# Optimization experiments

Hardware: AMD Instinct MI355X
Metric: run time of the kernel (lower is better)

The kernel has to match this reference:

```python
import jax, jax.numpy as jnp
import numpy as np

LMAX_IN = 3
LMAX_OUT = 3
C = 64          # num_channel
H = 64          # num_channel_hidden
N_NODES = 2048
N_EDGES = 8192

# All coupled (l1, l2, l3) paths with |l1-l2| <= l3 <= min(l1+l2, lmax_out)
COMBS = [(l1, l2, l3)
         for l1 in range(LMAX_IN + 1)
         for l2 in range(LMAX_OUT + 1)
         for l3 in range(abs(l1 - l2), min(l1 + l2, LMAX_OUT) + 1)]
COUNTS = {l3: sum(1 for c in COMBS if c[2] == l3) for l3 in range(LMAX_OUT + 1)}

# Fixed coupling (Clebsch-Gordan-like) tensors for each path, shape (2l1+1, 2l2+1, 2l3+1).
# Deterministic constants (not trained / not differentiated), standing in for the
# e3nn CG coefficients used by InterEinsumTC.
_rng = np.random.RandomState(1234)
CG = [jnp.asarray((_rng.randn(2 * l1 + 1, 2 * l2 + 1, 2 * l3 + 1) * 0.2).astype(np.float32))
      for (l1, l2, l3) in COMBS]


def setup_inputs() -> dict:
    key = jax.random.key(0)
    ks = jax.random.split(key, 16)
    inp = {}
    for l in range(LMAX_OUT + 1):
        inp[f"x{l}"] = jax.random.normal(ks[l], (N_NODES, C, 2 * l + 1), dtype=jnp.float32)
        inp[f"y{l}"] = jax.random.normal(ks[4 + l], (N_EDGES, 2 * l + 1), dtype=jnp.float32)
        fan_in = C * COUNTS[l]
        inp[f"w_lin{l}"] = jax.random.normal(ks[8 + l], (fan_in, H), dtype=jnp.float32) / np.float32(np.sqrt(fan_in))
    inp["ws"] = jax.random.normal(ks[12], (N_EDGES, C * len(COMBS)), dtype=jnp.float32)
    inp["edge_index"] = jax.random.randint(ks[13], (2, N_EDGES), 0, N_NODES, dtype=jnp.int32)
    return inp


def _forward(x0, x1, x2, x3, y0, y1, y2, y3, ws, w_lin0, w_lin1, w_lin2, w_lin3, edge_index):
    xs = (x0, x1, x2, x3)
    ys = (y0, y1, y2, y3)
    wl = (w_lin0, w_lin1, w_lin2, w_lin3)
    src, dst = edge_index[0], edge_index[1]
    # per-edge gather of node features for every input degree
    xg = [x[src] for x in xs]                      # [E, C, 2l1+1]
    buf = {l3: [] for l3 in range(LMAX_OUT + 1)}
    for i, (l1, l2, l3) in enumerate(COMBS):
        # tensor-product contraction: [E, C, 2l3+1]
        out = jnp.einsum('lmn,ecl,em->ecn', CG[i], xg[l1], ys[l2])
        w = ws[:, i * C:(i + 1) * C][:, :, None]   # [E, C, 1] per-path per-channel weight
        buf[l3].append(w * out)
    res = []
    for l3 in range(LMAX_OUT + 1):
        m_ji = jnp.concatenate(buf[l3], axis=1)    # [E, C*count_l3, 2l3+1]
        m_i = jax.ops.segment_sum(m_ji, dst, num_segments=N_NODES)  # scatter-sum -> [N, C*count, 2l3+1]
        res.append(jnp.einsum('ncm,ch->nhm', m_i, wl[l3]))          # per-l3 linear -> [N, H, 2l3+1]
    return tuple(res)


def reference(x0, x1, x2, x3, y0, y1, y2, y3, ws, w_lin0, w_lin1, w_lin2, w_lin3, edge_index):
    return _forward(x0, x1, x2, x3, y0, y1, y2, y3, ws,
                    w_lin0, w_lin1, w_lin2, w_lin3, edge_index)
```

## Files before the change

### kernel.cpp

```cpp
#include <hip/hip_runtime.h>
#include <hip/hip_bf16.h>
#include <cmath>
#include <cstdint>

#define NNODES 2048
#define NEDGES 8192
#define NCH 64
#define NHID 64
#define NPATH 34
#define NTASK (NPATH * NCH)
#define CGTOT 3436
#define MROW 9984
#define TT3 1028
#define EBLK 8
#define GLEN_MAX 564

#define MI_BYTES ((size_t)NNODES * MROW * 2)
#define XT_BYTES ((size_t)NNODES * 16 * NCH * 2)
#define WT_BYTES ((size_t)64 * NTASK * 2)
#define OFF_OFF  (MI_BYTES)
#define CUR_OFF  (OFF_OFF + 2052 * 4)
#define PACK_OFF (CUR_OFF + 2048 * 4)
#define ORD_OFF  (PACK_OFF + 8192 * 4)
#define XT_OFF   (ORD_OFF + 2048 * 4)
#define WT_OFF   (XT_OFF + XT_BYTES)
#define CGP_OFF  (WT_OFF + WT_BYTES)
#define CGP_FLOATS (TT3 * 9)

typedef __attribute__((ext_vector_type(8))) short short8;
typedef __attribute__((ext_vector_type(4))) float floatx4;

struct PathTables {
  int l1[NPATH], l2[NPATH], l3[NPATH];
  int cg_off[NPATH], t_off3[NPATH], rank[NPATH];
  int gpaths[2][20], gnp[2], gbase3[2], glen3[2];
  int cg_total, tt3, npaths;
};

constexpr PathTables make_tables() {
  PathTables tb{};
  int np = 0;
  for (int a = 0; a < 4; ++a)
    for (int b = 0; b < 4; ++b) {
      int lo = a > b ? a - b : b - a;
      int hi = a + b < 3 ? a + b : 3;
      for (int c = lo; c <= hi; ++c) { tb.l1[np] = a; tb.l2[np] = b; tb.l3[np] = c; ++np; }
    }
  int cg = 0;
  int cnt[4] = {0, 0, 0, 0};
  for (int i = 0; i < np; ++i) {
    tb.cg_off[i] = cg; tb.rank[i] = cnt[tb.l3[i]]++;
    cg += (2 * tb.l1[i] + 1) * (2 * tb.l2[i] + 1) * (2 * tb.l3[i] + 1);
  }
  int tt = 0;
  for (int g = 0; g < 2; ++g) {
    tb.gbase3[g] = tt;
    for (int i = 0; i < np; ++i) {
      int gi = (tb.l3[i] == 0 || tb.l3[i] == 3) ? 0 : 1;
      if (gi != g) continue;
      tb.gpaths[g][tb.gnp[g]++] = i;
      tb.t_off3[i] = tt;
      int d1 = 2 * tb.l1[i] + 1, d3 = 2 * tb.l3[i] + 1;
      int st = (d3 <= 4) ? 4 : 8;
      tt += d1 * st;
    }
    tb.glen3[g] = tt - tb.gbase3[g];
  }
  tb.cg_total = cg; tb.tt3 = tt; tb.npaths = np;
  return tb;
}

constexpr PathTables H_TB = make_tables();
static_assert(H_TB.npaths == NPATH, "npaths");
static_assert(H_TB.cg_total == CGTOT, "cgtot");
static_assert(H_TB.tt3 == TT3, "tt3");
static_assert(H_TB.gnp[0] == 14 && H_TB.gnp[1] == 20, "gnp");
static_assert(H_TB.gbase3[1] == 464 && H_TB.glen3[0] == 464 && H_TB.glen3[1] == 564, "gsplit");

__constant__ PathTables d_tb = make_tables();

namespace {
struct MT19937 {
  uint32_t mt[624]; int mti; bool has_g; double gval;
  void seed(uint32_t s) {
    for (int i = 0; i < 624; ++i) { mt[i] = s; s = 1812433253u * (s ^ (s >> 30)) + (uint32_t)i + 1u; }
    mti = 624; has_g = false; gval = 0.0;
  }
  uint32_t next() {
    if (mti >= 624) {
      for (int i = 0; i < 624; ++i) {
        uint32_t y = (mt[i] & 0x80000000u) | (mt[(i + 1) % 624] & 0x7fffffffu);
        mt[i] = mt[(i + 397) % 624] ^ (y >> 1) ^ ((y & 1u) ? 0x9908b0dfu : 0u);
      }
      mti = 0;
    }
    uint32_t y = mt[mti++];
    y ^= y >> 11; y ^= (y << 7) & 0x9d2c5680u; y ^= (y << 15) & 0xefc60000u; y ^= y >> 18;
    return y;
  }
  double rdbl() {
    uint32_t a = next() >> 5, b = next() >> 6;
    return ((double)a * 67108864.0 + (double)b) / 9007199254740992.0;
  }
  double gauss() {
    if (has_g) { has_g = false; return gval; }
    double x1, x2, r2;
    do {
      x1 = 2.0 * rdbl() - 1.0;
      x2 = 2.0 * rdbl() - 1.0;
      r2 = x1 * x1 + x2 * x2;
    } while (r2 >= 1.0 || r2 == 0.0);
    double f = std::sqrt(-2.0 * std::log(r2) / r2);
    gval = f * x1; has_g = true;
    return f * x2;
  }
};

float host_pack[CGP_FLOATS];
float* g_cg_dev = nullptr;
bool g_cg_ok = false;

struct CGInit {
  CGInit() {
    static float cg[CGTOT];
    MT19937 g; g.seed(1234u);
    int idx = 0;
    for (int i = 0; i < NPATH; ++i) {
      int d1 = 2 * H_TB.l1[i] + 1, d2 = 2 * H_TB.l2[i] + 1, d3 = 2 * H_TB.l3[i] + 1;
      int sz = d1 * d2 * d3;
      for (int k = 0; k < sz; ++k) cg[idx++] = (float)(g.gauss() * 0.2);
    }
    const int ybase[4] = {0, 1, 4, 9};
    for (int k = 0; k < CGP_FLOATS; ++k) host_pack[k] = 0.f;
    for (int i = 0; i < NPATH; ++i) {
      int d1 = 2 * H_TB.l1[i] + 1, d2 = 2 * H_TB.l2[i] + 1, d3 = 2 * H_TB.l3[i] + 1;
      int st = (d3 <= 4) ? 4 : 8;
      for (int l = 0; l < d1; ++l)
        for (int n3 = 0; n3 < d3; ++n3) {
          int slot = H_TB.t_off3[i] + l * st + n3;
          for (int m = 0; m < d2; ++m)
            host_pack[slot * 8 + m] = cg[H_TB.cg_off[i] + l * d2 * d3 + m * d3 + n3];
          host_pack[TT3 * 8 + slot] = (float)ybase[H_TB.l2[i]];
        }
    }
    (void)hipHostRegister(host_pack, sizeof(host_pack), hipHostRegisterDefault);
    void* p = nullptr;
    if (hipMalloc(&p, sizeof(host_pack)) == hipSuccess && p) {
      if (hipMemcpy(p, host_pack, sizeof(host_pack), hipMemcpyHostToDevice) == hipSuccess) {
        float back = -1.f;
        if (hipMemcpy(&back, (float*)p + (CGP_FLOATS - 1), sizeof(float),
                      hipMemcpyDeviceToHost) == hipSuccess && back == host_pack[CGP_FLOATS - 1]) {
          g_cg_dev = (float*)p;
          g_cg_ok = true;
        }
      }
    }
  }
} cg_init_instance;
}

__device__ __forceinline__ float bf2f(unsigned short u) {
  union { unsigned int i; float f; } v; v.i = ((unsigned int)u) << 16; return v.f;
}
__device__ __forceinline__ unsigned short f2bf(float f) {
  __hip_bfloat16 h = __float2bfloat16(f);
  union { __hip_bfloat16 h; unsigned short u; } v; v.h = h; return v.u;
}

__global__ __launch_bounds__(1024) void scan_kernel(
    const int* __restrict__ edge_index, int* __restrict__ off, int* __restrict__ cursor,
    int* __restrict__ order)
{
  __shared__ int ldeg[NNODES];
  __shared__ int csum[1024];
  __shared__ int hist[64];
  const int t = threadIdx.x;
  for (int i = t; i < NNODES; i += 1024) ldeg[i] = 0;
  __syncthreads();
  const int* __restrict__ dsts = edge_index + NEDGES;
  for (int e = t; e < NEDGES; e += 1024) atomicAdd(&ldeg[dsts[e]], 1);
  __syncthreads();
  const int l0 = ldeg[2 * t], l1 = ldeg[2 * t + 1];
  const int s = l0 + l1;
  csum[t] = s;
  __syncthreads();
  for (int o = 1; o < 1024; o <<= 1) {
    int v = (t >= o) ? csum[t - o] : 0;
    __syncthreads();
    csum[t] += v;
    __syncthreads();
  }
  int run = csum[t] - s;
  off[2 * t] = run; cursor[2 * t] = run;
  off[2 * t + 1] = run + l0; cursor[2 * t + 1] = run + l0;
  if (t == 0) off[NNODES] = NEDGES;
  if (t < 64) hist[t] = 0;
  __syncthreads();
  for (int i = t; i < NNODES; i += 1024) {
    int d = ldeg[i]; d = d > 63 ? 63 : d;
    atomicAdd(&hist[63 - d], 1);
  }
  __syncthreads();
  if (t == 0) { int r2 = 0; for (int b = 0; b < 64; ++b) { int c = hist[b]; hist[b] = r2; r2 += c; } }
  __syncthreads();
  for (int i = t; i < NNODES; i += 1024) {
    int d = ldeg[i]; d = d > 63 ? 63 : d;
    int pos = atomicAdd(&hist[63 - d], 1);
    order[pos] = i;
  }
}

__global__ __launch_bounds__(256) void fill_xt_kernel(
    const int* __restrict__ edge_index, int* __restrict__ cursor, int* __restrict__ pack,
    const float* __restrict__ x0, const float* __restrict__ x1,
    const float* __restrict__ x2, const float* __restrict__ x3,
    const float* __restrict__ wl0, const float* __restrict__ wl1,
    const float* __restrict__ wl2, const float* __restrict__ wl3,
    __hip_bfloat16* __restrict__ xT, unsigned short* __restrict__ wt_all)
{
  const int b = blockIdx.x;
  const int t = threadIdx.x;
  if (b < 32) {
    const int e = b * 256 + t;
    const int d = edge_index[NEDGES + e];
    const int s = edge_index[e];
    const int pos = atomicAdd(&cursor[d], 1);
    pack[pos] = e | (s << 13);
  } else if (b < 32 + NNODES) {
    const int n = b - 32;
    for (int idx = t; idx < 1024; idx += 256) {
      const int j = idx >> 6, c = idx & 63;
      const float* src; int d1, m;
      if (j < 1)      { src = x0; d1 = 1; m = j; }
      else if (j < 4) { src = x1; d1 = 3; m = j - 1; }
      else if (j < 9) { src = x2; d1 = 5; m = j - 4; }
      else            { src = x3; d1 = 7; m = j - 9; }
      const float v = src[((size_t)n * NCH + c) * d1 + m];
      xT[((size_t)n * 16 + j) * NCH + c] = __float2bfloat16(v);
    }
  } else {
    const int b3 = b - (32 + NNODES);
    const int k = b3 * 4 + (t >> 6);
    const int h = t & 63;
    const float* src; int K, base, kl;
    if (k < 256)       { src = wl0; K = 256; base = 0;     kl = k; }
    else if (k < 832)  { src = wl1; K = 576; base = 16384; kl = k - 256; }
    else if (k < 1536) { src = wl2; K = 704; base = 53248; kl = k - 832; }
    else               { src = wl3; K = 640; base = 98304; kl = k - 1536; }
    wt_all[base + h * K + kl] = f2bf(src[(size_t)kl * 64 + h]);
  }
}

template <int D1, int D3>
__device__ __forceinline__ void tp_task_run(
    int wcol, int toff_l, int rank, int nb, const int* __restrict__ epk,
    const float (*Ts)[GLEN_MAX], const float* __restrict__ ws,
    const unsigned short* __restrict__ xT,
    int n, bool first, __hip_bfloat16* __restrict__ m_out)
{
  constexpr int Kc = (D3 == 1) ? 256 : (D3 == 3) ? 576 : (D3 == 5) ? 704 : 640;
  constexpr int Rc = (D3 == 1) ? 0 : (D3 == 3) ? 256 : (D3 == 5) ? 1984 : 5504;
  constexpr int JB = (D1 == 1) ? 0 : (D1 == 3) ? 1 : (D1 == 5) ? 4 : 9;
  constexpr int ST = (D3 <= 4) ? 4 : 8;
  const int c = wcol & 63;

  float wv_[EBLK];
#pragma unroll
  for (int ei = 0; ei < EBLK; ++ei)
    wv_[ei] = (ei < nb) ? ws[(size_t)(epk[ei] & 8191) * NTASK + wcol] : 0.f;

  float acc[D3];
#pragma unroll
  for (int m = 0; m < D3; ++m) acc[m] = 0.f;

  for (int ei = 0; ei < nb; ++ei) {
    const int s = epk[ei] >> 13;
    const unsigned short* __restrict__ xr = xT + ((size_t)s * 16 + JB) * NCH + c;
    const float* __restrict__ Tp = &Ts[ei][toff_l];
    float u[D3];
#pragma unroll
    for (int m = 0; m < D3; ++m) u[m] = 0.f;
#pragma unroll
    for (int l = 0; l < D1; ++l) {
      const float xv = bf2f(xr[l * NCH]);
      const floatx4 r0 = *(const floatx4*)(Tp + l * ST);
      floatx4 r1;
      if (D3 > 4) r1 = *(const floatx4*)(Tp + l * ST + 4);
#pragma unroll
      for (int m = 0; m < D3; ++m)
        u[m] += xv * ((m < 4) ? r0[m] : r1[m - 4]);
    }
#pragma unroll
    for (int m = 0; m < D3; ++m) acc[m] += wv_[ei] * u[m];
  }

  __hip_bfloat16* mo = m_out + (size_t)n * MROW + Rc + rank * NCH + c;
  if (first) {
#pragma unroll
    for (int m = 0; m < D3; ++m) mo[m * Kc] = __float2bfloat16(acc[m]);
  } else {
#pragma unroll
    for (int m = 0; m < D3; ++m)
      mo[m * Kc] = __float2bfloat16(__bfloat162float(mo[m * Kc]) + acc[m]);
  }
}

__global__ __launch_bounds__(256) void tp_node_kernel(
    const float* __restrict__ y0, const float* __restrict__ y1,
    const float* __restrict__ y2, const float* __restrict__ y3,
    const float* __restrict__ ws, const unsigned short* __restrict__ xT,
    const float* __restrict__ cg_pack,
    const int* __restrict__ off, const int* __restrict__ pack,
    const int* __restrict__ order,
    __hip_bfloat16* __restrict__ m_out)
{
  __shared__ float Ts[EBLK][GLEN_MAX];
  __shared__ float y_s[EBLK][18];
  __shared__ int epk[EBLK];

  const int bid = blockIdx.x;
  const int n = order[bid >> 1];
  const int g = bid & 1;
  const int t = threadIdx.x;
  const int beg = off[n];
  const int cnt = off[n + 1] - beg;
  const int gbase = d_tb.gbase3[g];
  const int glen  = d_tb.glen3[g];
  const int ntask = d_tb.gnp[g] << 6;
  const float* __restrict__ metaf = cg_pack + TT3 * 8;

  for (int base = 0; base == 0 || base < cnt; base += EBLK) {
    int nb = cnt - base;
    nb = nb < 0 ? 0 : (nb > EBLK ? EBLK : nb);
    if (t < nb) epk[t] = pack[beg + base + t];
    if (t >= 64 && t < 64 + 2 * EBLK) y_s[(t - 64) >> 1][16 + (t & 1)] = 0.f;
    __syncthreads();
    if (t < nb * 16) {
      const int ei = t >> 4, j = t & 15;
      const int e = epk[ei] & 8191;
      float v;
      if (j < 1)      v = y0[e];
      else if (j < 4) v = y1[e * 3 + (j - 1)];
      else if (j < 9) v = y2[e * 5 + (j - 4)];
      else            v = y3[e * 7 + (j - 9)];
      y_s[ei][j] = v;
    }
    __syncthreads();
    for (int ei = 0; ei < nb; ++ei) {
      for (int j = t; j < glen; j += 256) {
        const int slot = gbase + j;
        const float4 a = *(const float4*)(cg_pack + slot * 8);
        const float4 c4 = *(const float4*)(cg_pack + slot * 8 + 4);
        const int yb = (int)metaf[slot];
        const float* yy = &y_s[ei][yb];
        Ts[ei][j] = a.x * yy[0] + a.y * yy[1] + a.z * yy[2] + a.w * yy[3]
                  + c4.x * yy[4] + c4.y * yy[5] + c4.z * yy[6] + c4.w * yy[7];
      }
    }
    __syncthreads();

    const bool first = (base == 0);
    for (int k = 0; k * 256 + t < ntask; ++k) {
      const int tl = k * 256 + t;
      const int i = d_tb.gpaths[g][tl >> 6];
      const int wcol = (i << 6) | (tl & 63);
      const int toff_l = d_tb.t_off3[i] - gbase;
      const int rk = d_tb.rank[i];
      const int code = d_tb.l1[i] * 4 + d_tb.l3[i];
      switch (code) {
        case  0: tp_task_run<1,1>(wcol, toff_l, rk, nb, epk, Ts, ws, xT, n, first, m_out); break;
        case  1: tp_task_run<1,3>(wcol, toff_l, rk, nb, epk, Ts, ws, xT, n, first, m_out); break;
        case  2: tp_task_run<1,5>(wcol, toff_l, rk, nb, epk, Ts, ws, xT, n, first, m_out); break;
        case  3: tp_task_run<1,7>(wcol, toff_l, rk, nb, epk, Ts, ws, xT, n, first, m_out); break;
        case  4: tp_task_run<3,1>(wcol, toff_l, rk, nb, epk, Ts, ws, xT, n, first, m_out); break;
        case  5: tp_task_run<3,3>(wcol, toff_l, rk, nb, epk, Ts, ws, xT, n, first, m_out); break;
        case  6: tp_task_run<3,5>(wcol, toff_l, rk, nb, epk, Ts, ws, xT, n, first, m_out); break;
        case  7: tp_task_run<3,7>(wcol, toff_l, rk, nb, epk, Ts, ws, xT, n, first, m_out); break;
        case  8: tp_task_run<5,1>(wcol, toff_l, rk, nb, epk, Ts, ws, xT, n, first, m_out); break;
        case  9: tp_task_run<5,3>(wcol, toff_l, rk, nb, epk, Ts, ws, xT, n, first, m_out); break;
        case 10: tp_task_run<5,5>(wcol, toff_l, rk, nb, epk, Ts, ws, xT, n, first, m_out); break;
        case 11: tp_task_run<5,7>(wcol, toff_l, rk, nb, epk, Ts, ws, xT, n, first, m_out); break;
        case 12: tp_task_run<7,1>(wcol, toff_l, rk, nb, epk, Ts, ws, xT, n, first, m_out); break;
        case 13: tp_task_run<7,3>(wcol, toff_l, rk, nb, epk, Ts, ws, xT, n, first, m_out); break;
        case 14: tp_task_run<7,5>(wcol, toff_l, rk, nb, epk, Ts, ws, xT, n, first, m_out); break;
        default: tp_task_run<7,7>(wcol, toff_l, rk, nb, epk, Ts, ws, xT, n, first, m_out); break;
      }
    }
    __syncthreads();
  }
}

template <int D3, int K, int ROFF>
__device__ __forceinline__ void lin_mfma_body(
    int blk, const unsigned short* __restrict__ mu, const unsigned short* __restrict__ wt,
    float* __restrict__ out)
{
  const int t = threadIdx.x;
  const int wv = t >> 6;
  const int lane = t & 63;
  const int idx16 = lane & 15;
  const int quad = lane >> 4;

  const int arow = blk * 64 + wv * 16 + idx16;
  const int ann = arow / D3, amm = arow - ann * D3;
  const unsigned short* __restrict__ ap = mu + (size_t)ann * MROW + ROFF + amm * K + quad * 8;
  const unsigned short* __restrict__ bp = wt + idx16 * K + quad * 8;

  floatx4 acc[4] = {{0.f,0.f,0.f,0.f},{0.f,0.f,0.f,0.f},{0.f,0.f,0.f,0.f},{0.f,0.f,0.f,0.f}};

  for (int k0 = 0; k0 < K; k0 += 32) {
    const short8 af = *(const short8*)(ap + k0);
#pragma unroll
    for (int nt = 0; nt < 4; ++nt) {
      const short8 bf = *(const short8*)(bp + nt * 16 * K + k0);
      acc[nt] = __builtin_amdgcn_mfma_f32_16x16x32_bf16(af, bf, acc[nt], 0, 0, 0);
    }
  }

#pragma unroll
  for (int nt = 0; nt < 4; ++nt) {
    const int h = nt * 16 + idx16;
#pragma unroll
    for (int r = 0; r < 4; ++r) {
      const int row = blk * 64 + wv * 16 + quad * 4 + r;
      const int nn = row / D3, mm = row - nn * D3;
      out[((size_t)nn * NHID + h) * D3 + mm] = acc[nt][r];
    }
  }
}

__global__ __launch_bounds__(256) void lin_fused_kernel(
    const unsigned short* __restrict__ mu, const unsigned short* __restrict__ wt_all,
    float* __restrict__ out)
{
  const int b = blockIdx.x;
  if (b < 32)       lin_mfma_body<1, 256, 0>   (b,       mu, wt_all,         out);
  else if (b < 128) lin_mfma_body<3, 576, 256> (b - 32,  mu, wt_all + 16384, out + 131072);
  else if (b < 288) lin_mfma_body<5, 704, 1984>(b - 128, mu, wt_all + 53248, out + 524288);
  else              lin_mfma_body<7, 640, 5504>(b - 288, mu, wt_all + 98304, out + 1179648);
}

extern "C" void kernel_launch(void* const* d_in, const int* in_sizes, int n_in,
                              void* d_out, int out_size, void* d_ws, size_t ws_size,
                              hipStream_t stream) {
  const float* x0  = (const float*)d_in[0];
  const float* y0  = (const float*)d_in[1];
  const float* wl0 = (const float*)d_in[2];
  const float* x1  = (const float*)d_in[3];
  const float* y1  = (const float*)d_in[4];
  const float* wl1 = (const float*)d_in[5];
  const float* x2  = (const float*)d_in[6];
  const float* y2  = (const float*)d_in[7];
  const float* wl2 = (const float*)d_in[8];
  const float* x3  = (const float*)d_in[9];
  const float* y3  = (const float*)d_in[10];
  const float* wl3 = (const float*)d_in[11];
  const float* ws  = (const float*)d_in[12];
  const int* edge_index = (const int*)d_in[13];
  float* out = (float*)d_out;

  __hip_bfloat16* m_i = (__hip_bfloat16*)d_ws;
  int* csr_off = (int*)((char*)d_ws + OFF_OFF);
  int* cursor  = (int*)((char*)d_ws + CUR_OFF);
  int* pack    = (int*)((char*)d_ws + PACK_OFF);
  int* order   = (int*)((char*)d_ws + ORD_OFF);
  __hip_bfloat16* xT = (__hip_bfloat16*)((char*)d_ws + XT_OFF);
  unsigned short* wt_all = (unsigned short*)((char*)d_ws + WT_OFF);

  const float* cg_pack;
  if (g_cg_ok) {
    cg_pack = g_cg_dev;
  } else {
    float* cg_ws = (float*)((char*)d_ws + CGP_OFF);
    hipMemcpyAsync(cg_ws, host_pack, sizeof(host_pack), hipMemcpyHostToDevice, stream);
    cg_pack = cg_ws;
  }

  scan_kernel<<<1, 1024, 0, stream>>>(edge_index, csr_off, cursor, order);
  fill_xt_kernel<<<32 + NNODES + 544, 256, 0, stream>>>(edge_index, cursor, pack,
                                                        x0, x1, x2, x3,
                                                        wl0, wl1, wl2, wl3,
                                                        xT, wt_all);
  tp_node_kernel<<<2 * NNODES, 256, 0, stream>>>(y0, y1, y2, y3, ws,
                                                 (const unsigned short*)xT, cg_pack,
                                                 csr_off, pack, order, m_i);
  lin_fused_kernel<<<512, 256, 0, stream>>>((const unsigned short*)m_i, wt_all, out);
}
```

Measured before the change: 244.0 us.

## Fuse node linear layer into tensor-product kernel via LDS-staged messages

```diff
diff --git a/kernel.cpp b/kernel.cpp
--- a/kernel.cpp
+++ b/kernel.cpp
@@ -10,21 +10,17 @@
 #define NPATH 34
 #define NTASK (NPATH * NCH)
 #define CGTOT 3436
-#define MROW 9984
 #define TT3 1028
 #define EBLK 8
 #define GLEN_MAX 564
-
-#define MI_BYTES ((size_t)NNODES * MROW * 2)
-#define XT_BYTES ((size_t)NNODES * 16 * NCH * 2)
-#define WT_BYTES ((size_t)64 * NTASK * 2)
-#define OFF_OFF  (MI_BYTES)
-#define CUR_OFF  (OFF_OFF + 2052 * 4)
-#define PACK_OFF (CUR_OFF + 2048 * 4)
-#define ORD_OFF  (PACK_OFF + 8192 * 4)
-#define XT_OFF   (ORD_OFF + 2048 * 4)
-#define WT_OFF   (XT_OFF + XT_BYTES)
-#define CGP_OFF  (WT_OFF + WT_BYTES)
+#define MST_SIZE 5312
+
+#define OFF_OFF  0
+#define PACK_OFF 16384
+#define ORD_OFF  65536
+#define XT_OFF   131072
+#define WT_OFF   (XT_OFF + (size_t)NNODES * 16 * NCH * 2)
+#define CGP_OFF  (WT_OFF + (size_t)64 * NTASK * 2)
 #define CGP_FLOATS (TT3 * 9)
 
 typedef __attribute__((ext_vector_type(8))) short short8;
@@ -167,20 +163,21 @@
   union { __hip_bfloat16 h; unsigned short u; } v; v.h = h; return v.u;
 }
 
-__global__ __launch_bounds__(1024) void scan_kernel(
-    const int* __restrict__ edge_index, int* __restrict__ off, int* __restrict__ cursor,
-    int* __restrict__ order)
-{
-  __shared__ int ldeg[NNODES];
+__global__ __launch_bounds__(1024) void scan_fill_kernel(
+    const int* __restrict__ edge_index, int* __restrict__ off,
+    int* __restrict__ pack, int* __restrict__ order)
+{
+  __shared__ int lcur[NNODES];
   __shared__ int csum[1024];
   __shared__ int hist[64];
   const int t = threadIdx.x;
-  for (int i = t; i < NNODES; i += 1024) ldeg[i] = 0;
-  __syncthreads();
+  for (int i = t; i < NNODES; i += 1024) lcur[i] = 0;
+  __syncthreads();
+  const int* __restrict__ srcs = edge_index;
   const int* __restrict__ dsts = edge_index + NEDGES;
-  for (int e = t; e < NEDGES; e += 1024) atomicAdd(&ldeg[dsts[e]], 1);
-  __syncthreads();
-  const int l0 = ldeg[2 * t], l1 = ldeg[2 * t + 1];
+  for (int e = t; e < NEDGES; e += 1024) atomicAdd(&lcur[dsts[e]], 1);
+  __syncthreads();
+  const int l0 = lcur[2 * t], l1 = lcur[2 * t + 1];
   const int s = l0 + l1;
   csum[t] = s;
   __syncthreads();
@@ -190,56 +187,67 @@
     csum[t] += v;
     __syncthreads();
   }
-  int run = csum[t] - s;
-  off[2 * t] = run; cursor[2 * t] = run;
-  off[2 * t + 1] = run + l0; cursor[2 * t + 1] = run + l0;
+  const int run = csum[t] - s;
+  off[2 * t] = run;
+  off[2 * t + 1] = run + l0;
   if (t == 0) off[NNODES] = NEDGES;
   if (t < 64) hist[t] = 0;
   __syncthreads();
-  for (int i = t; i < NNODES; i += 1024) {
-    int d = ldeg[i]; d = d > 63 ? 63 : d;
-    atomicAdd(&hist[63 - d], 1);
+  {
+    int d0 = l0 > 63 ? 63 : l0, d1 = l1 > 63 ? 63 : l1;
+    atomicAdd(&hist[63 - d0], 1);
+    atomicAdd(&hist[63 - d1], 1);
   }
   __syncthreads();
   if (t == 0) { int r2 = 0; for (int b = 0; b < 64; ++b) { int c = hist[b]; hist[b] = r2; r2 += c; } }
   __syncthreads();
-  for (int i = t; i < NNODES; i += 1024) {
-    int d = ldeg[i]; d = d > 63 ? 63 : d;
-    int pos = atomicAdd(&hist[63 - d], 1);
-    order[pos] = i;
-  }
-}
-
-__global__ __launch_bounds__(256) void fill_xt_kernel(
-    const int* __restrict__ edge_index, int* __restrict__ cursor, int* __restrict__ pack,
+  {
+    int d0 = l0 > 63 ? 63 : l0, d1 = l1 > 63 ? 63 : l1;
+    int p0 = atomicAdd(&hist[63 - d0], 1); order[p0] = 2 * t;
+    int p1 = atomicAdd(&hist[63 - d1], 1); order[p1] = 2 * t + 1;
+  }
+  lcur[2 * t] = run;
+  lcur[2 * t + 1] = run + l0;
+  __syncthreads();
+  for (int e = t; e < NEDGES; e += 1024) {
+    const int d = dsts[e];
+    const int pos = atomicAdd(&lcur[d], 1);
+    pack[pos] = e | (srcs[e] << 13);
+  }
+}
+
+__global__ __launch_bounds__(256) void xt_wt_kernel(
     const float* __restrict__ x0, const float* __restrict__ x1,
     const float* __restrict__ x2, const float* __restrict__ x3,
     const float* __restrict__ wl0, const float* __restrict__ wl1,
     const float* __restrict__ wl2, const float* __restrict__ wl3,
-    __hip_bfloat16* __restrict__ xT, unsigned short* __restrict__ wt_all)
+    unsigned short* __restrict__ xT, unsigned short* __restrict__ wt_all)
 {
   const int b = blockIdx.x;
   const int t = threadIdx.x;
-  if (b < 32) {
-    const int e = b * 256 + t;
-    const int d = edge_index[NEDGES + e];
-    const int s = edge_index[e];
-    const int pos = atomicAdd(&cursor[d], 1);
-    pack[pos] = e | (s << 13);
-  } else if (b < 32 + NNODES) {
-    const int n = b - 32;
+  if (b < NNODES) {
+    __shared__ float xs[1024];
+    const int n = b;
+    for (int j = t; j < 1024; j += 256) {
+      float v;
+      if (j < 64)       v = x0[(size_t)n * 64 + j];
+      else if (j < 256) v = x1[(size_t)n * 192 + (j - 64)];
+      else if (j < 576) v = x2[(size_t)n * 320 + (j - 256)];
+      else              v = x3[(size_t)n * 448 + (j - 576)];
+      xs[j] = v;
+    }
+    __syncthreads();
     for (int idx = t; idx < 1024; idx += 256) {
       const int j = idx >> 6, c = idx & 63;
-      const float* src; int d1, m;
-      if (j < 1)      { src = x0; d1 = 1; m = j; }
-      else if (j < 4) { src = x1; d1 = 3; m = j - 1; }
-      else if (j < 9) { src = x2; d1 = 5; m = j - 4; }
-      else            { src = x3; d1 = 7; m = j - 9; }
-      const float v = src[((size_t)n * NCH + c) * d1 + m];
-      xT[((size_t)n * 16 + j) * NCH + c] = __float2bfloat16(v);
+      float v;
+      if (j < 1)      v = xs[c];
+      else if (j < 4) v = xs[64 + c * 3 + (j - 1)];
+      else if (j < 9) v = xs[256 + c * 5 + (j - 4)];
+      else            v = xs[576 + c * 7 + (j - 9)];
+      xT[((size_t)n * 16 + j) * NCH + c] = f2bf(v);
     }
   } else {
-    const int b3 = b - (32 + NNODES);
+    const int b3 = b - NNODES;
     const int k = b3 * 4 + (t >> 6);
     const int h = t & 63;
     const float* src; int K, base, kl;
@@ -252,14 +260,11 @@
 }
 
 template <int D1, int D3>
-__device__ __forceinline__ void tp_task_run(
-    int wcol, int toff_l, int rank, int nb, const int* __restrict__ epk,
+__device__ __forceinline__ void tp_acc_run(
+    int wcol, int toff_l, int nb, const int* __restrict__ epk,
     const float (*Ts)[GLEN_MAX], const float* __restrict__ ws,
-    const unsigned short* __restrict__ xT,
-    int n, bool first, __hip_bfloat16* __restrict__ m_out)
-{
-  constexpr int Kc = (D3 == 1) ? 256 : (D3 == 3) ? 576 : (D3 == 5) ? 704 : 640;
-  constexpr int Rc = (D3 == 1) ? 0 : (D3 == 3) ? 256 : (D3 == 5) ? 1984 : 5504;
+    const unsigned short* __restrict__ xT, float* __restrict__ acc)
+{
   constexpr int JB = (D1 == 1) ? 0 : (D1 == 3) ? 1 : (D1 == 5) ? 4 : 9;
   constexpr int ST = (D3 <= 4) ? 4 : 8;
   const int c = wcol & 63;
@@ -268,10 +273,6 @@
 #pragma unroll
   for (int ei = 0; ei < EBLK; ++ei)
     wv_[ei] = (ei < nb) ? ws[(size_t)(epk[ei] & 8191) * NTASK + wcol] : 0.f;
-
-  float acc[D3];
-#pragma unroll
-  for (int m = 0; m < D3; ++m) acc[m] = 0.f;
 
   for (int ei = 0; ei < nb; ++ei) {
     const int s = epk[ei] >> 13;
@@ -293,29 +294,61 @@
 #pragma unroll
     for (int m = 0; m < D3; ++m) acc[m] += wv_[ei] * u[m];
   }
-
-  __hip_bfloat16* mo = m_out + (size_t)n * MROW + Rc + rank * NCH + c;
-  if (first) {
-#pragma unroll
-    for (int m = 0; m < D3; ++m) mo[m * Kc] = __float2bfloat16(acc[m]);
-  } else {
-#pragma unroll
-    for (int m = 0; m < D3; ++m)
-      mo[m * Kc] = __float2bfloat16(__bfloat162float(mo[m * Kc]) + acc[m]);
-  }
-}
-
-__global__ __launch_bounds__(256) void tp_node_kernel(
+}
+
+template <int D3>
+__device__ __forceinline__ void store_task(
+    int wcol, int rank, const float* __restrict__ acc, unsigned short* __restrict__ mstage)
+{
+  constexpr int Kc = (D3 == 1) ? 256 : (D3 == 3) ? 576 : (D3 == 5) ? 704 : 640;
+  constexpr int SK = Kc + 8;
+  constexpr int MB = (D3 == 1) ? 0 : (D3 == 3) ? 0 : (D3 == 5) ? 1752 : 264;
+  const int c = wcol & 63;
+  unsigned short* mo = mstage + MB + rank * NCH + c;
+#pragma unroll
+  for (int m = 0; m < D3; ++m) mo[m * SK] = f2bf(acc[m]);
+}
+
+template <int M, int K>
+__device__ __forceinline__ void lin_node(
+    const unsigned short* __restrict__ mst, const unsigned short* __restrict__ wt,
+    float* __restrict__ outb, int n, int t)
+{
+  constexpr int SK = K + 8;
+  const int wv = t >> 6;
+  const int lane = t & 63;
+  const int idx16 = lane & 15;
+  const int quad = lane >> 4;
+  const unsigned short* __restrict__ bp = wt + (size_t)(wv * 16 + idx16) * K + quad * 8;
+  const unsigned short* __restrict__ ap = mst + idx16 * SK + quad * 8;
+
+  floatx4 acc = {0.f, 0.f, 0.f, 0.f};
+  for (int k0 = 0; k0 < K; k0 += 32) {
+    short8 af = {0, 0, 0, 0, 0, 0, 0, 0};
+    if (idx16 < M) af = *(const short8*)(ap + k0);
+    const short8 bf = *(const short8*)(bp + k0);
+    acc = __builtin_amdgcn_mfma_f32_16x16x32_bf16(af, bf, acc, 0, 0, 0);
+  }
+  const int h = wv * 16 + idx16;
+#pragma unroll
+  for (int r = 0; r < 4; ++r) {
+    const int m = quad * 4 + r;
+    if (m < M) outb[((size_t)n * NHID + h) * M + m] = acc[r];
+  }
+}
+
+__global__ __launch_bounds__(256) void fused_kernel(
     const float* __restrict__ y0, const float* __restrict__ y1,
     const float* __restrict__ y2, const float* __restrict__ y3,
     const float* __restrict__ ws, const unsigned short* __restrict__ xT,
     const float* __restrict__ cg_pack,
     const int* __restrict__ off, const int* __restrict__ pack,
-    const int* __restrict__ order,
-    __hip_bfloat16* __restrict__ m_out)
+    const int* __restrict__ order, const unsigned short* __restrict__ wt_all,
+    float* __restrict__ out)
 {
   __shared__ float Ts[EBLK][GLEN_MAX];
   __shared__ float y_s[EBLK][18];
+  __shared__ unsigned short mstage[MST_SIZE];
   __shared__ int epk[EBLK];
 
   const int bid = blockIdx.x;
@@ -329,6 +362,12 @@
   const int ntask = d_tb.gnp[g] << 6;
   const float* __restrict__ metaf = cg_pack + TT3 * 8;
 
+  float acc[5][7];
+#pragma unroll
+  for (int a = 0; a < 5; ++a)
+#pragma unroll
+    for (int m = 0; m < 7; ++m) acc[a][m] = 0.f;
+
   for (int base = 0; base == 0 || base < cnt; base += EBLK) {
     int nb = cnt - base;
     nb = nb < 0 ? 0 : (nb > EBLK ? EBLK : nb);
@@ -359,85 +398,61 @@
     }
     __syncthreads();
 
-    const bool first = (base == 0);
-    for (int k = 0; k * 256 + t < ntask; ++k) {
-      const int tl = k * 256 + t;
+#pragma unroll
+    for (int st = 0; st < 5; ++st) {
+      const int tl = st * 256 + t;
+      if (tl < ntask) {
+        const int i = d_tb.gpaths[g][tl >> 6];
+        const int wcol = (i << 6) | (tl & 63);
+        const int toff_l = d_tb.t_off3[i] - gbase;
+        const int code = d_tb.l1[i] * 4 + d_tb.l3[i];
+        switch (code) {
+          case  0: tp_acc_run<1,1>(wcol, toff_l, nb, epk, Ts, ws, xT, acc[st]); break;
+          case  1: tp_acc_run<1,3>(wcol, toff_l, nb, epk, Ts, ws, xT, acc[st]); break;
+          case  2: tp_acc_run<1,5>(wcol, toff_l, nb, epk, Ts, ws, xT, acc[st]); break;
+          case  3: tp_acc_run<1,7>(wcol, toff_l, nb, epk, Ts, ws, xT, acc[st]); break;
+          case  4: tp_acc_run<3,1>(wcol, toff_l, nb, epk, Ts, ws, xT, acc[st]); break;
+          case  5: tp_acc_run<3,3>(wcol, toff_l, nb, epk, Ts, ws, xT, acc[st]); break;
+          case  6: tp_acc_run<3,5>(wcol, toff_l, nb, epk, Ts, ws, xT, acc[st]); break;
+          case  7: tp_acc_run<3,7>(wcol, toff_l, nb, epk, Ts, ws, xT, acc[st]); break;
+          case  8: tp_acc_run<5,1>(wcol, toff_l, nb, epk, Ts, ws, xT, acc[st]); break;
+          case  9: tp_acc_run<5,3>(wcol, toff_l, nb, epk, Ts, ws, xT, acc[st]); break;
+          case 10: tp_acc_run<5,5>(wcol, toff_l, nb, epk, Ts, ws, xT, acc[st]); break;
+          case 11: tp_acc_run<5,7>(wcol, toff_l, nb, epk, Ts, ws, xT, acc[st]); break;
+          case 12: tp_acc_run<7,1>(wcol, toff_l, nb, epk, Ts, ws, xT, acc[st]); break;
+          case 13: tp_acc_run<7,3>(wcol, toff_l, nb, epk, Ts, ws, xT, acc[st]); break;
+          case 14: tp_acc_run<7,5>(wcol, toff_l, nb, epk, Ts, ws, xT, acc[st]); break;
+          default: tp_acc_run<7,7>(wcol, toff_l, nb, epk, Ts, ws, xT, acc[st]); break;
+        }
+      }
+    }
+    __syncthreads();
+  }
+
+#pragma unroll
+  for (int st = 0; st < 5; ++st) {
+    const int tl = st * 256 + t;
+    if (tl < ntask) {
       const int i = d_tb.gpaths[g][tl >> 6];
       const int wcol = (i << 6) | (tl & 63);
-      const int toff_l = d_tb.t_off3[i] - gbase;
       const int rk = d_tb.rank[i];
-      const int code = d_tb.l1[i] * 4 + d_tb.l3[i];
-      switch (code) {
-        case  0: tp_task_run<1,1>(wcol, toff_l, rk, nb, epk, Ts, ws, xT, n, first, m_out); break;
-        case  1: tp_task_run<1,3>(wcol, toff_l, rk, nb, epk, Ts, ws, xT, n, first, m_out); break;
-        case  2: tp_task_run<1,5>(wcol, toff_l, rk, nb, epk, Ts, ws, xT, n, first, m_out); break;
-        case  3: tp_task_run<1,7>(wcol, toff_l, rk, nb, epk, Ts, ws, xT, n, first, m_out); break;
-        case  4: tp_task_run<3,1>(wcol, toff_l, rk, nb, epk, Ts, ws, xT, n, first, m_out); break;
-        case  5: tp_task_run<3,3>(wcol, toff_l, rk, nb, epk, Ts, ws, xT, n, first, m_out); break;
-        case  6: tp_task_run<3,5>(wcol, toff_l, rk, nb, epk, Ts, ws, xT, n, first, m_out); break;
-        case  7: tp_task_run<3,7>(wcol, toff_l, rk, nb, epk, Ts, ws, xT, n, first, m_out); break;
-        case  8: tp_task_run<5,1>(wcol, toff_l, rk, nb, epk, Ts, ws, xT, n, first, m_out); break;
-        case  9: tp_task_run<5,3>(wcol, toff_l, rk, nb, epk, Ts, ws, xT, n, first, m_out); break;
-        case 10: tp_task_run<5,5>(wcol, toff_l, rk, nb, epk, Ts, ws, xT, n, first, m_out); break;
-        case 11: tp_task_run<5,7>(wcol, toff_l, rk, nb, epk, Ts, ws, xT, n, first, m_out); break;
-        case 12: tp_task_run<7,1>(wcol, toff_l, rk, nb, epk, Ts, ws, xT, n, first, m_out); break;
-        case 13: tp_task_run<7,3>(wcol, toff_l, rk, nb, epk, Ts, ws, xT, n, first, m_out); break;
-        case 14: tp_task_run<7,5>(wcol, toff_l, rk, nb, epk, Ts, ws, xT, n, first, m_out); break;
-        default: tp_task_run<7,7>(wcol, toff_l, rk, nb, epk, Ts, ws, xT, n, first, m_out); break;
+      switch (d_tb.l3[i]) {
+        case 0:  store_task<1>(wcol, rk, acc[st], mstage); break;
+        case 1:  store_task<3>(wcol, rk, acc[st], mstage); break;
+        case 2:  store_task<5>(wcol, rk, acc[st], mstage); break;
+        default: store_task<7>(wcol, rk, acc[st], mstage); break;
       }
     }
-    __syncthreads();
-  }
-}
-
-template <int D3, int K, int ROFF>
-__device__ __forceinline__ void lin_mfma_body(
-    int blk, const unsigned short* __restrict__ mu, const unsigned short* __restrict__ wt,
-    float* __restrict__ out)
-{
-  const int t = threadIdx.x;
-  const int wv = t >> 6;
-  const int lane = t & 63;
-  const int idx16 = lane & 15;
-  const int quad = lane >> 4;
-
-  const int arow = blk * 64 + wv * 16 + idx16;
-  const int ann = arow / D3, amm = arow - ann * D3;
-  const unsigned short* __restrict__ ap = mu + (size_t)ann * MROW + ROFF + amm * K + quad * 8;
-  const unsigned short* __restrict__ bp = wt + idx16 * K + quad * 8;
-
-  floatx4 acc[4] = {{0.f,0.f,0.f,0.f},{0.f,0.f,0.f,0.f},{0.f,0.f,0.f,0.f},{0.f,0.f,0.f,0.f}};
-
-  for (int k0 = 0; k0 < K; k0 += 32) {
-    const short8 af = *(const short8*)(ap + k0);
-#pragma unroll
-    for (int nt = 0; nt < 4; ++nt) {
-      const short8 bf = *(const short8*)(bp + nt * 16 * K + k0);
-      acc[nt] = __builtin_amdgcn_mfma_f32_16x16x32_bf16(af, bf, acc[nt], 0, 0, 0);
-    }
-  }
-
-#pragma unroll
-  for (int nt = 0; nt < 4; ++nt) {
-    const int h = nt * 16 + idx16;
-#pragma unroll
-    for (int r = 0; r < 4; ++r) {
-      const int row = blk * 64 + wv * 16 + quad * 4 + r;
-      const int nn = row / D3, mm = row - nn * D3;
-      out[((size_t)nn * NHID + h) * D3 + mm] = acc[nt][r];
-    }
-  }
-}
-
-__global__ __launch_bounds__(256) void lin_fused_kernel(
-    const unsigned short* __restrict__ mu, const unsigned short* __restrict__ wt_all,
-    float* __restrict__ out)
-{
-  const int b = blockIdx.x;
-  if (b < 32)       lin_mfma_body<1, 256, 0>   (b,       mu, wt_all,         out);
-  else if (b < 128) lin_mfma_body<3, 576, 256> (b - 32,  mu, wt_all + 16384, out + 131072);
-  else if (b < 288) lin_mfma_body<5, 704, 1984>(b - 128, mu, wt_all + 53248, out + 524288);
-  else              lin_mfma_body<7, 640, 5504>(b - 288, mu, wt_all + 98304, out + 1179648);
+  }
+  __syncthreads();
+
+  if (g == 0) {
+    lin_node<1, 256>(mstage,        wt_all,         out,           n, t);
+    lin_node<7, 640>(mstage + 264,  wt_all + 98304, out + 1179648, n, t);
+  } else {
+    lin_node<3, 576>(mstage,        wt_all + 16384, out + 131072,  n, t);
+    lin_node<5, 704>(mstage + 1752, wt_all + 53248, out + 524288,  n, t);
+  }
 }
 
 extern "C" void kernel_launch(void* const* d_in, const int* in_sizes, int n_in,
@@ -459,12 +474,10 @@
   const int* edge_index = (const int*)d_in[13];
   float* out = (float*)d_out;
 
-  __hip_bfloat16* m_i = (__hip_bfloat16*)d_ws;
   int* csr_off = (int*)((char*)d_ws + OFF_OFF);
-  int* cursor  = (int*)((char*)d_ws + CUR_OFF);
   int* pack    = (int*)((char*)d_ws + PACK_OFF);
   int* order   = (int*)((char*)d_ws + ORD_OFF);
-  __hip_bfloat16* xT = (__hip_bfloat16*)((char*)d_ws + XT_OFF);
+  unsigned short* xT     = (unsigned short*)((char*)d_ws + XT_OFF);
   unsigned short* wt_all = (unsigned short*)((char*)d_ws + WT_OFF);
 
   const float* cg_pack;
@@ -476,13 +489,9 @@
     cg_pack = cg_ws;
   }
 
-  scan_kernel<<<1, 1024, 0, stream>>>(edge_index, csr_off, cursor, order);
-  fill_xt_kernel<<<32 + NNODES + 544, 256, 0, stream>>>(edge_index, cursor, pack,
-                                                        x0, x1, x2, x3,
-                                                        wl0, wl1, wl2, wl3,
-                                                        xT, wt_all);
-  tp_node_kernel<<<2 * NNODES, 256, 0, stream>>>(y0, y1, y2, y3, ws,
-                                                 (const unsigned short*)xT, cg_pack,
-                                                 csr_off, pack, order, m_i);
-  lin_fused_kernel<<<512, 256, 0, stream>>>((const unsigned short*)m_i, wt_all, out);
-}
+  scan_fill_kernel<<<1, 1024, 0, stream>>>(edge_index, csr_off, pack, order);
+  xt_wt_kernel<<<NNODES + 544, 256, 0, stream>>>(x0, x1, x2, x3,
+                                                 wl0, wl1, wl2, wl3, xT, wt_all);
+  fused_kernel<<<2 * NNODES, 256, 0, stream>>>(y0, y1, y2, y3, ws, xT, cg_pack,
+                                               csr_off, pack, order, wt_all, out);
+}
```

After: 315.4 us. +29.2%, slower.
